# Performance work log

Measured on AMD Instinct MI355X. Metric: run time of the kernel, lower is better.

## Reference

```python
import jax, jax.numpy as jnp
import numpy as np

NUM_ITERATIONS = 3
EPS = 1e-7

def squash(v, axis=-1):
    # scale = |v|^2/(1+|v|^2) * v/sqrt(|v|^2+eps), matching the torch module
    sq = jnp.sum(v * v, axis=axis, keepdims=True)
    return (sq / (1.0 + sq)) * v / jnp.sqrt(sq + EPS)

def setup_inputs() -> dict:
    key = jax.random.key(0)
    kx, kw = jax.random.split(key)
    B, R, C, O, I = 256, 1152, 10, 16, 8
    x = jax.random.normal(kx, (B, R, I), dtype=jnp.float32)
    W = jax.random.normal(kw, (R, C, O, I), dtype=jnp.float32)
    return {"x": x, "W": W}

def reference(x, W):
    B, R, I = x.shape
    C, O = W.shape[1], W.shape[2]
    # u_hat[b,r,c,o] = sum_i W[r,c,o,i] * x[b,r,i]  (batched tiny GEMV)
    u_hat = jnp.einsum('rcoi,bri->brco', W, x)
    b_ij = jnp.zeros((B, R, C), dtype=u_hat.dtype)
    v = None
    for it in range(NUM_ITERATIONS):
        c_ij = jax.nn.softmax(b_ij, axis=1)          # softmax over route nodes (dim=1, as in source)
        s_j = jnp.einsum('brc,brco->bco', c_ij, u_hat)
        v = squash(s_j, axis=-1)                      # squash over out_channels (dim=-2 of the 5D torch tensor)
        if it != NUM_ITERATIONS - 1:
            b_ij = b_ij + jnp.einsum('brco,bco->brc', u_hat, v)
    # match torch output shape (B, 1, C, O, 1)
    return v[:, None, :, :, None]
```

## Files before the change

kernel.cpp:

```cpp
#include <hip/hip_runtime.h>
#include <cstdint>

#define BB 256
#define RR 1152
#define CC 10
#define OO 16
#define II 8
#define NT 768
#define GG 4
#define NWAVE (NT / 64)
#define WPG (NWAVE / GG)
#define LOG2E 1.4426950408889634f

typedef float float2v __attribute__((ext_vector_type(2)));

__device__ __forceinline__ void unpack2(uint32_t pk, float& lo, float& hi) {
    union { uint32_t i; float f; } a, b;
    a.i = pk << 16; b.i = pk & 0xffff0000u;
    lo = a.f; hi = b.f;
}
__device__ __forceinline__ float dot4pk(float4 a, float4 b) {
    float2v al = { a.x, a.y }, ah = { a.z, a.w };
    float2v bl = { b.x, b.y }, bh = { b.z, b.w };
    float2v h = __builtin_elementwise_fma(ah, bh, al * bl);
    return h.x + h.y;
}
__device__ __forceinline__ float qpadd1(float v) {
    int o = __builtin_amdgcn_mov_dpp(__float_as_int(v), 0xB1, 0xF, 0xF, true);
    return v + __int_as_float(o);
}
__device__ __forceinline__ float qpadd2(float v) {
    int o = __builtin_amdgcn_mov_dpp(__float_as_int(v), 0x4E, 0xF, 0xF, true);
    return v + __int_as_float(o);
}
__device__ __forceinline__ float dppx2f(float v) {
    return __int_as_float(__builtin_amdgcn_mov_dpp(__float_as_int(v), 0x4E, 0xF, 0xF, true));
}
__device__ __forceinline__ uint32_t cvtpk(float lo, float hi) {
    uint32_t r;
    asm("v_cvt_pk_bf16_f32 %0, %1, %2" : "=v"(r) : "v"(lo), "v"(hi));
    return r;
}
#if __has_builtin(__builtin_amdgcn_exp2f)
#define EXP2(x) __builtin_amdgcn_exp2f(x)
#else
#define EXP2(x) __expf((x) * 0.6931471805599453f)
#endif
#define LD4(P) (*reinterpret_cast<const float4*>(P))

#define P1G(XV, SG0, SG1, SG2, SG3, WR)                                       \
  do {                                                                        \
    float d0 = qpadd1(dot4pk(w0, XV));                                        \
    float d1 = qpadd1(dot4pk(w1, XV));                                        \
    float d2 = qpadd1(dot4pk(w2, XV));                                        \
    float d3 = qpadd1(dot4pk(w3, XV));                                        \
    SG0 += d0; SG1 += d1; SG2 += d2; SG3 += d3;                               \
    float sa = pb1 ? (pb0 ? d3 : d2) : (pb0 ? d1 : d0);                       \
    float sb = pb1 ? (pb0 ? d1 : d0) : (pb0 ? d3 : d2);                       \
    (WR)[(size_t)it * 768] = cvtpk(sa, dppx2f(sb));                           \
  } while (0)

__global__ __launch_bounds__(NT, 3)
void k_caps(const float* __restrict__ x, const float* __restrict__ W,
            float* __restrict__ out) {
    extern __shared__ uint32_t u2[];
    __shared__ float part[NWAVE][17];
    __shared__ float p0s[NWAVE][8][4][GG];
    __shared__ float wsum[GG][OO];

    const int t = threadIdx.x;
    const int c  = blockIdx.x / (BB / GG);
    const int b0 = (blockIdx.x % (BB / GG)) * GG;
    const int wv = t >> 6, l = t & 63;
    const int rg = t >> 3, p = t & 7;

    uint32_t* uA = u2;
    uint32_t* uB = u2 + (size_t)RR * 8;
    uint32_t* uC = u2 + (size_t)2 * RR * 8;
    uint32_t* uD = u2 + (size_t)3 * RR * 8;

    const int pos = (p >> 1) + ((p & 1) << 2);
    uint32_t* wrA = uA + (size_t)rg * 8 + pos;
    uint32_t* wrB = uB + (size_t)rg * 8 + pos;
    uint32_t* wrC = uC + (size_t)rg * 8 + pos;
    uint32_t* wrD = uD + (size_t)rg * 8 + pos;
    const bool pb0 = (p & 1) != 0, pb1 = (p & 2) != 0;

    float s00 = 0.f, s01 = 0.f, s02 = 0.f, s03 = 0.f;
    float s10 = 0.f, s11 = 0.f, s12 = 0.f, s13 = 0.f;
    float s20 = 0.f, s21 = 0.f, s22 = 0.f, s23 = 0.f;
    float s30 = 0.f, s31 = 0.f, s32 = 0.f, s33 = 0.f;
#pragma unroll 2
    for (int it = 0; it < 12; ++it) {
        const int r = it * 96 + rg;
        const float* wrow = W + ((size_t)r * CC + c) * (OO * II) + p * 4;
        float4 w0 = LD4(wrow);
        float4 w1 = LD4(wrow + 32);
        float4 w2 = LD4(wrow + 64);
        float4 w3 = LD4(wrow + 96);
        const float* xp = x + ((size_t)b0 * RR + r) * II + (p & 1) * 4;
        float4 xa = LD4(xp);
        float4 xb = LD4(xp + (size_t)RR * II);
        float4 xc = LD4(xp + (size_t)2 * RR * II);
        float4 xd = LD4(xp + (size_t)3 * RR * II);
        P1G(xa, s00, s01, s02, s03, wrA);
        P1G(xb, s10, s11, s12, s13, wrB);
        P1G(xc, s20, s21, s22, s23, wrC);
        P1G(xd, s30, s31, s32, s33, wrD);
    }
#pragma unroll
    for (int m = 8; m < 64; m <<= 1) {
        s00 += __shfl_xor(s00, m); s01 += __shfl_xor(s01, m);
        s02 += __shfl_xor(s02, m); s03 += __shfl_xor(s03, m);
        s10 += __shfl_xor(s10, m); s11 += __shfl_xor(s11, m);
        s12 += __shfl_xor(s12, m); s13 += __shfl_xor(s13, m);
        s20 += __shfl_xor(s20, m); s21 += __shfl_xor(s21, m);
        s22 += __shfl_xor(s22, m); s23 += __shfl_xor(s23, m);
        s30 += __shfl_xor(s30, m); s31 += __shfl_xor(s31, m);
        s32 += __shfl_xor(s32, m); s33 += __shfl_xor(s33, m);
    }
    if (l < 8) {
        p0s[wv][l][0][0] = s00; p0s[wv][l][1][0] = s01;
        p0s[wv][l][2][0] = s02; p0s[wv][l][3][0] = s03;
        p0s[wv][l][0][1] = s10; p0s[wv][l][1][1] = s11;
        p0s[wv][l][2][1] = s12; p0s[wv][l][3][1] = s13;
        p0s[wv][l][0][2] = s20; p0s[wv][l][1][2] = s21;
        p0s[wv][l][2][2] = s22; p0s[wv][l][3][2] = s23;
        p0s[wv][l][0][3] = s30; p0s[wv][l][1][3] = s31;
        p0s[wv][l][2][3] = s32; p0s[wv][l][3][3] = s33;
    }
    __syncthreads();

    if (t < GG * OO) {
        const int g = t >> 4, o = t & 15;
        float s = 0.f;
#pragma unroll
        for (int w = 0; w < NWAVE; ++w) s += p0s[w][2 * (o & 3)][o >> 2][g];
        s *= (1.0f / RR);
        float ss = s * s;
        ss += __shfl_xor(ss, 1); ss += __shfl_xor(ss, 2);
        ss += __shfl_xor(ss, 4); ss += __shfl_xor(ss, 8);
        wsum[g][o] = s * (ss / ((1.0f + ss) * sqrtf(ss + 1e-7f)));
    }
    __syncthreads();

    const int g2 = wv / WPG;
    const int wv3 = wv - g2 * WPG;
    const uint32_t* ug = u2 + (size_t)g2 * RR * 8;
    const int q = l & 3;
    const int rl = l >> 2;
    const int rbase = wv3 * 16 + rl;
    const uint32_t* rp = ug + (size_t)rbase * 8 + 2 * q;

    for (int pass = 1; pass < 3; ++pass) {
        const float2v WQA = { wsum[g2][2 * q] * LOG2E,
                              wsum[g2][2 * q + 8] * LOG2E };
        const float2v WQB = { wsum[g2][2 * q + 1] * LOG2E,
                              wsum[g2][2 * q + 9] * LOG2E };
        float2v N0 = { 0.f, 0.f }, N1 = { 0.f, 0.f };
        float den = 0.f;

#pragma unroll
        for (int it2 = 0; it2 < 24; ++it2) {
            uint2 pp = *reinterpret_cast<const uint2*>(rp + (size_t)it2 * 384);
            float2v P0, P1;
            {
                float u0, u1, u2f, u3;
                unpack2(pp.x, u0, u1);
                unpack2(pp.y, u3, u2f);
                P0.x = u0; P0.y = u2f;
                P1.x = u1; P1.y = u3;
            }
            float2v lg2 = __builtin_elementwise_fma(P0, WQA, P1 * WQB);
            float lg = lg2.x + lg2.y;
            lg = qpadd1(lg);
            lg = qpadd2(lg);
            float e = EXP2(lg);
            den += e;
            float2v E2 = { e, e };
            N0 = __builtin_elementwise_fma(E2, P0, N0);
            N1 = __builtin_elementwise_fma(E2, P1, N1);
        }

        float n0 = N0.x, n2 = N0.y, n1 = N1.x, n3 = N1.y;
#pragma unroll
        for (int m = 4; m < 64; m <<= 1) {
            n0 += __shfl_xor(n0, m); n1 += __shfl_xor(n1, m);
            n2 += __shfl_xor(n2, m); n3 += __shfl_xor(n3, m);
            den += __shfl_xor(den, m);
        }
        if (l < 4) {
            part[wv][2 * l]     = n0;
            part[wv][2 * l + 1] = n1;
            part[wv][2 * l + 8] = n2;
            part[wv][2 * l + 9] = n3;
            if (l == 0) part[wv][16] = den;
        }
        __syncthreads();

        if (t < GG * OO) {
            const int g = t >> 4, o = t & 15;
            float nf = 0.f, df = 0.f;
#pragma unroll
            for (int w = 0; w < WPG; ++w) {
                nf += part[WPG * g + w][o];
                df += part[WPG * g + w][16];
            }
            float s = nf / df;
            float ss = s * s;
            ss += __shfl_xor(ss, 1); ss += __shfl_xor(ss, 2);
            ss += __shfl_xor(ss, 4); ss += __shfl_xor(ss, 8);
            float v = s * (ss / ((1.0f + ss) * sqrtf(ss + 1e-7f)));
            if (pass == 2)
                out[((size_t)(b0 + g) * CC + c) * OO + o] = v;
            else
                wsum[g][o] += v;
        }
        __syncthreads();
    }
}

extern "C" void kernel_launch(void* const* d_in, const int* in_sizes, int n_in,
                              void* d_out, int out_size, void* d_ws, size_t ws_size,
                              hipStream_t stream) {
    const float* x = (const float*)d_in[0];
    const float* W = (const float*)d_in[1];
    if (n_in >= 2 && in_sizes[0] == RR * CC * OO * II &&
        in_sizes[1] == BB * RR * II) {
        const float* tmp = x; x = W; W = tmp;
    }
    float* out = (float*)d_out;

    const size_t dyn_lds = (size_t)GG * RR * 8 * 4;
    static bool s_attr = false;
    if (!s_attr) {
        hipFuncSetAttribute(reinterpret_cast<const void*>(k_caps),
                            hipFuncAttributeMaxDynamicSharedMemorySize,
                            (int)dyn_lds);
        s_attr = true;
    }
    k_caps<<<CC * (BB / GG), NT, dyn_lds, stream>>>(x, W, out);
}
```

Measured before the change: 114.2 us.

## Halve batch group per block and replace shared-memory broadcasts with redundant wave-level squash

The block now handles 2 batch elements instead of 4, which halves dynamic LDS (72KB) and doubles the grid, with launch bounds raised to allow more resident blocks per CU. Every wave now redundantly computes the squash and routing-weight update itself, using shuffles instead of a single-thread-group write to shared wsum. This removes one __syncthreads per pass and the serialized section. Partial sums are double-buffered by pass parity to avoid a trailing barrier. W reuse across batch elements drops, so W global/L2 traffic doubles, and the extra work is paid redundantly by every wave.

```diff
diff --git a/kernel.cpp b/kernel.cpp
--- a/kernel.cpp
+++ b/kernel.cpp
@@ -7,7 +7,7 @@
 #define OO 16
 #define II 8
 #define NT 768
-#define GG 4
+#define GG 2
 #define NWAVE (NT / 64)
 #define WPG (NWAVE / GG)
 #define LOG2E 1.4426950408889634f
@@ -60,13 +60,12 @@
     (WR)[(size_t)it * 768] = cvtpk(sa, dppx2f(sb));                           \
   } while (0)
 
-__global__ __launch_bounds__(NT, 3)
+__global__ __launch_bounds__(NT, 6)
 void k_caps(const float* __restrict__ x, const float* __restrict__ W,
             float* __restrict__ out) {
     extern __shared__ uint32_t u2[];
-    __shared__ float part[NWAVE][17];
     __shared__ float p0s[NWAVE][8][4][GG];
-    __shared__ float wsum[GG][OO];
+    __shared__ float part2[2][17][NWAVE];
 
     const int t = threadIdx.x;
     const int c  = blockIdx.x / (BB / GG);
@@ -76,20 +75,14 @@
 
     uint32_t* uA = u2;
     uint32_t* uB = u2 + (size_t)RR * 8;
-    uint32_t* uC = u2 + (size_t)2 * RR * 8;
-    uint32_t* uD = u2 + (size_t)3 * RR * 8;
 
     const int pos = (p >> 1) + ((p & 1) << 2);
     uint32_t* wrA = uA + (size_t)rg * 8 + pos;
     uint32_t* wrB = uB + (size_t)rg * 8 + pos;
-    uint32_t* wrC = uC + (size_t)rg * 8 + pos;
-    uint32_t* wrD = uD + (size_t)rg * 8 + pos;
     const bool pb0 = (p & 1) != 0, pb1 = (p & 2) != 0;
 
     float s00 = 0.f, s01 = 0.f, s02 = 0.f, s03 = 0.f;
     float s10 = 0.f, s11 = 0.f, s12 = 0.f, s13 = 0.f;
-    float s20 = 0.f, s21 = 0.f, s22 = 0.f, s23 = 0.f;
-    float s30 = 0.f, s31 = 0.f, s32 = 0.f, s33 = 0.f;
 #pragma unroll 2
     for (int it = 0; it < 12; ++it) {
         const int r = it * 96 + rg;
@@ -101,12 +94,8 @@
         const float* xp = x + ((size_t)b0 * RR + r) * II + (p & 1) * 4;
         float4 xa = LD4(xp);
         float4 xb = LD4(xp + (size_t)RR * II);
-        float4 xc = LD4(xp + (size_t)2 * RR * II);
-        float4 xd = LD4(xp + (size_t)3 * RR * II);
         P1G(xa, s00, s01, s02, s03, wrA);
         P1G(xb, s10, s11, s12, s13, wrB);
-        P1G(xc, s20, s21, s22, s23, wrC);
-        P1G(xd, s30, s31, s32, s33, wrD);
     }
 #pragma unroll
     for (int m = 8; m < 64; m <<= 1) {
@@ -114,63 +103,57 @@
         s02 += __shfl_xor(s02, m); s03 += __shfl_xor(s03, m);
         s10 += __shfl_xor(s10, m); s11 += __shfl_xor(s11, m);
         s12 += __shfl_xor(s12, m); s13 += __shfl_xor(s13, m);
-        s20 += __shfl_xor(s20, m); s21 += __shfl_xor(s21, m);
-        s22 += __shfl_xor(s22, m); s23 += __shfl_xor(s23, m);
-        s30 += __shfl_xor(s30, m); s31 += __shfl_xor(s31, m);
-        s32 += __shfl_xor(s32, m); s33 += __shfl_xor(s33, m);
     }
     if (l < 8) {
         p0s[wv][l][0][0] = s00; p0s[wv][l][1][0] = s01;
         p0s[wv][l][2][0] = s02; p0s[wv][l][3][0] = s03;
         p0s[wv][l][0][1] = s10; p0s[wv][l][1][1] = s11;
         p0s[wv][l][2][1] = s12; p0s[wv][l][3][1] = s13;
-        p0s[wv][l][0][2] = s20; p0s[wv][l][1][2] = s21;
-        p0s[wv][l][2][2] = s22; p0s[wv][l][3][2] = s23;
-        p0s[wv][l][0][3] = s30; p0s[wv][l][1][3] = s31;
-        p0s[wv][l][2][3] = s32; p0s[wv][l][3][3] = s33;
     }
     __syncthreads();
 
-    if (t < GG * OO) {
-        const int g = t >> 4, o = t & 15;
-        float s = 0.f;
-#pragma unroll
-        for (int w = 0; w < NWAVE; ++w) s += p0s[w][2 * (o & 3)][o >> 2][g];
-        s *= (1.0f / RR);
-        float ss = s * s;
+    const int g2 = wv / WPG;
+    const int wv6 = wv - g2 * WPG;
+    const uint32_t* ug = g2 ? uB : uA;
+    const int q = l & 3;
+    const int rl = l >> 2;
+    const int rbase = wv6 * 16 + rl;
+    const uint32_t* rp = ug + (size_t)rbase * 8 + 2 * q;
+
+    const int oo = l & 15;
+    const int gb = l & 48;
+    const int t0 = gb | (2 * q), t1 = gb | (2 * q + 1);
+    const int t2 = gb | (2 * q + 8), t3 = gb | (2 * q + 9);
+
+    float ra, rb, rc, rd;
+    {
+        float sv = 0.f;
+#pragma unroll
+        for (int w = 0; w < NWAVE; ++w) sv += p0s[w][2 * (oo & 3)][oo >> 2][g2];
+        sv *= (1.0f / RR);
+        float ss = sv * sv;
         ss += __shfl_xor(ss, 1); ss += __shfl_xor(ss, 2);
         ss += __shfl_xor(ss, 4); ss += __shfl_xor(ss, 8);
-        wsum[g][o] = s * (ss / ((1.0f + ss) * sqrtf(ss + 1e-7f)));
-    }
-    __syncthreads();
-
-    const int g2 = wv / WPG;
-    const int wv3 = wv - g2 * WPG;
-    const uint32_t* ug = u2 + (size_t)g2 * RR * 8;
-    const int q = l & 3;
-    const int rl = l >> 2;
-    const int rbase = wv3 * 16 + rl;
-    const uint32_t* rp = ug + (size_t)rbase * 8 + 2 * q;
-
+        float vv = sv * (ss / ((1.0f + ss) * sqrtf(ss + 1e-7f)));
+        ra = __shfl(vv, t0); rb = __shfl(vv, t1);
+        rc = __shfl(vv, t2); rd = __shfl(vv, t3);
+    }
+
+#pragma unroll
     for (int pass = 1; pass < 3; ++pass) {
-        const float2v WQA = { wsum[g2][2 * q] * LOG2E,
-                              wsum[g2][2 * q + 8] * LOG2E };
-        const float2v WQB = { wsum[g2][2 * q + 1] * LOG2E,
-                              wsum[g2][2 * q + 9] * LOG2E };
+        const float2v WQA = { ra * LOG2E, rc * LOG2E };
+        const float2v WQB = { rb * LOG2E, rd * LOG2E };
         float2v N0 = { 0.f, 0.f }, N1 = { 0.f, 0.f };
         float den = 0.f;
 
 #pragma unroll
-        for (int it2 = 0; it2 < 24; ++it2) {
-            uint2 pp = *reinterpret_cast<const uint2*>(rp + (size_t)it2 * 384);
-            float2v P0, P1;
-            {
-                float u0, u1, u2f, u3;
-                unpack2(pp.x, u0, u1);
-                unpack2(pp.y, u3, u2f);
-                P0.x = u0; P0.y = u2f;
-                P1.x = u1; P1.y = u3;
-            }
+        for (int it2 = 0; it2 < 12; ++it2) {
+            uint2 pp = *reinterpret_cast<const uint2*>(rp + (size_t)it2 * 768);
+            float u0, u1, u2f, u3;
+            unpack2(pp.x, u0, u1);
+            unpack2(pp.y, u3, u2f);
+            float2v P0 = { u0, u2f };
+            float2v P1 = { u1, u3 };
             float2v lg2 = __builtin_elementwise_fma(P0, WQA, P1 * WQB);
             float lg = lg2.x + lg2.y;
             lg = qpadd1(lg);
@@ -189,34 +172,37 @@
             n2 += __shfl_xor(n2, m); n3 += __shfl_xor(n3, m);
             den += __shfl_xor(den, m);
         }
+        const int pb = pass & 1;
         if (l < 4) {
-            part[wv][2 * l]     = n0;
-            part[wv][2 * l + 1] = n1;
-            part[wv][2 * l + 8] = n2;
-            part[wv][2 * l + 9] = n3;
-            if (l == 0) part[wv][16] = den;
+            part2[pb][2 * l][wv]     = n0;
+            part2[pb][2 * l + 1][wv] = n1;
+            part2[pb][2 * l + 8][wv] = n2;
+            part2[pb][2 * l + 9][wv] = n3;
+            if (l == 0) part2[pb][16][wv] = den;
         }
         __syncthreads();
 
-        if (t < GG * OO) {
-            const int g = t >> 4, o = t & 15;
-            float nf = 0.f, df = 0.f;
-#pragma unroll
-            for (int w = 0; w < WPG; ++w) {
-                nf += part[WPG * g + w][o];
-                df += part[WPG * g + w][16];
-            }
-            float s = nf / df;
-            float ss = s * s;
-            ss += __shfl_xor(ss, 1); ss += __shfl_xor(ss, 2);
-            ss += __shfl_xor(ss, 4); ss += __shfl_xor(ss, 8);
-            float v = s * (ss / ((1.0f + ss) * sqrtf(ss + 1e-7f)));
-            if (pass == 2)
-                out[((size_t)(b0 + g) * CC + c) * OO + o] = v;
-            else
-                wsum[g][o] += v;
-        }
-        __syncthreads();
+        const float* po = &part2[pb][oo][0];
+        const float* pd = &part2[pb][16][0];
+        float nf = 0.f, df = 0.f;
+#pragma unroll
+        for (int w = 0; w < WPG; ++w) {
+            nf += po[g2 * WPG + w];
+            df += pd[g2 * WPG + w];
+        }
+        float s2 = nf / df;
+        float ss2 = s2 * s2;
+        ss2 += __shfl_xor(ss2, 1); ss2 += __shfl_xor(ss2, 2);
+        ss2 += __shfl_xor(ss2, 4); ss2 += __shfl_xor(ss2, 8);
+        float vv2 = s2 * (ss2 / ((1.0f + ss2) * sqrtf(ss2 + 1e-7f)));
+
+        if (pass == 1) {
+            ra += __shfl(vv2, t0); rb += __shfl(vv2, t1);
+            rc += __shfl(vv2, t2); rd += __shfl(vv2, t3);
+        } else {
+            if ((wv == 0 || wv == WPG) && l < 16)
+                out[((size_t)(b0 + g2) * CC + c) * OO + oo] = vv2;
+        }
     }
 }
 
@@ -232,12 +218,5 @@
     float* out = (float*)d_out;
 
     const size_t dyn_lds = (size_t)GG * RR * 8 * 4;
-    static bool s_attr = false;
-    if (!s_attr) {
-        hipFuncSetAttribute(reinterpret_cast<const void*>(k_caps),
-                            hipFuncAttributeMaxDynamicSharedMemorySize,
-                            (int)dyn_lds);
-        s_attr = true;
-    }
     k_caps<<<CC * (BB / GG), NT, dyn_lds, stream>>>(x, W, out);
 }
```

Result: faster. 109.7 us (-3.9%).
